# Optimization experiments

Hardware: AMD Instinct MI355X
Metric: run time of the kernel (lower is better)

## Reference

```python
import jax, jax.numpy as jnp
import numpy as np

jax.config.update("jax_enable_x64", True)

P = 2013265921          # NTT-friendly prime 15 * 2**27 + 1 (int64-safe proxy for BLS12-377 Fr)
GEN = 31                # generator of the multiplicative group of F_P
LOGN = 22
N = 1 << LOGN           # domain_size
C = 4                   # columns, as in the module docstring example


def _pow_table(base, n):
    """powers[k] = base**k mod P for k in [0, n), built by repeated doubling (vectorized)."""
    pw = np.ones(n, dtype=np.int64)
    cur = base % P
    step = 1
    while step < n:
        hi = min(2 * step, n)
        pw[step:hi] = (pw[:hi - step] * cur) % P
        cur = (cur * cur) % P
        step *= 2
    return pw


def setup_inputs() -> dict:
    key = jax.random.key(0)
    x = jax.random.randint(key, (N, C), 0, P, dtype=jnp.int64)
    omega = pow(GEN, (P - 1) // N, P)          # primitive N-th root of unity
    omega_inv = pow(omega, P - 2, P)           # its inverse (Fermat)
    twiddles = jnp.asarray(_pow_table(omega_inv, N // 2))  # omega_inv**k, k < N/2  (the 'Params' table)
    n_inv = jnp.asarray(pow(N, P - 2, P), dtype=jnp.int64)  # N^{-1} mod P
    return {"input": x, "twiddles": twiddles, "n_inv": n_inv}


def reference(input, twiddles, n_inv):
    """Inverse NTT over F_P, columns transformed independently. Output in natural order."""
    n, c = input.shape
    logn = n.bit_length() - 1
    # bit-reversal permutation indices (static; computed with numpy)
    idx = np.arange(n)
    rev = np.zeros(n, dtype=np.int64)
    for i in range(logn):
        rev = (rev << 1) | ((idx >> i) & 1)
    x = input[rev]
    # iterative Cooley-Tukey butterflies, logn stages
    for s in range(1, logn + 1):
        m = 1 << s
        half = m >> 1
        w = twiddles[:: n // m]                 # [half] = omega_inv**(j * n/m)
        xr = x.reshape(-1, m, c)                # [n/m, m, c]
        lo, hi = xr[:, :half], xr[:, half:]
        t = (w[None, :, None] * hi) % P         # modular twiddle multiply
        x = jnp.concatenate([(lo + t) % P, (lo - t) % P], axis=1).reshape(n, c)
    return (x * n_inv) % P                      # scale by N^{-1}
```

## Files before the change

kernel.cpp:

```cpp
#include <hip/hip_runtime.h>
#include <stdint.h>

static constexpr uint32_t P = 2013265921u;
static constexpr int      LOGM = 11;
static constexpr int      MSZ  = 1 << LOGM;
static constexpr int      NCOL = 4;

__host__ __device__ constexpr uint32_t neg_pinv32() {
    uint32_t x = 1u;
    for (int i = 0; i < 5; ++i) x *= 2u - P * x;
    return 0u - x;
}
static constexpr uint32_t NEG_PINV = neg_pinv32();
static constexpr uint32_t R1 = (uint32_t)(((uint64_t)1 << 32) % P);
static constexpr uint32_t R2 = (uint32_t)(((uint64_t)R1 * R1) % P);

__device__ __forceinline__ uint32_t mont_mul(uint32_t a, uint32_t b) {
    uint64_t t = (uint64_t)a * (uint64_t)b;
    uint32_t m = (uint32_t)t * NEG_PINV;
    uint32_t r = (uint32_t)((t + (uint64_t)m * P) >> 32);
    uint32_t s = r - P;
    return s < r ? s : r;
}
__device__ __forceinline__ uint32_t to_mont(uint32_t a) { return mont_mul(a, R2); }
__device__ __forceinline__ uint32_t add_p(uint32_t a, uint32_t b) {
    uint32_t r = a + b, s = r - P; return s < r ? s : r;
}
__device__ __forceinline__ uint32_t sub_p(uint32_t a, uint32_t b) {
    uint32_t r = a - b, s = r + P; return s < r ? s : r;
}
__device__ __forceinline__ uint4 mm4(uint32_t w, uint4 v) {
    return make_uint4(mont_mul(w, v.x), mont_mul(w, v.y),
                      mont_mul(w, v.z), mont_mul(w, v.w));
}
__device__ __forceinline__ void bf4(uint4& L, uint4& H, uint32_t w) {
    uint4 t = mm4(w, H);
    uint4 l = L;
    L = make_uint4(add_p(l.x, t.x), add_p(l.y, t.y), add_p(l.z, t.z), add_p(l.w, t.w));
    H = make_uint4(sub_p(l.x, t.x), sub_p(l.y, t.y), sub_p(l.z, t.z), sub_p(l.w, t.w));
}

__device__ __forceinline__ int g_sw(int el) {
    return el ^ (((el >> 3) ^ (el >> 6)) & 7);
}
__device__ __forceinline__ int fidx(int el, int c) { return (g_sw(el) << 2) | c; }

__device__ __forceinline__ void radix8(uint4 x[8],
        uint32_t ta, uint32_t tb0, uint32_t tb1,
        uint32_t tc0, uint32_t tc1, uint32_t tc2, uint32_t tc3) {
    bf4(x[0], x[1], ta);  bf4(x[2], x[3], ta);
    bf4(x[4], x[5], ta);  bf4(x[6], x[7], ta);
    bf4(x[0], x[2], tb0); bf4(x[1], x[3], tb1);
    bf4(x[4], x[6], tb0); bf4(x[5], x[7], tb1);
    bf4(x[0], x[4], tc0); bf4(x[1], x[5], tc1);
    bf4(x[2], x[6], tc2); bf4(x[3], x[7], tc3);
}

template <bool PASS2>
__global__ __launch_bounds__(1024, 4) void intt_pass(
        const uint4* __restrict__ src, uint4* __restrict__ dst,
        const uint32_t* __restrict__ tw,
        const uint32_t* __restrict__ ninv_p)
{
    __shared__ uint4    buf[MSZ * NCOL];
    __shared__ uint32_t stab[2048];

    const int      t   = threadIdx.x;
    const int      c4  = t & 3;
    const int      sub = t >> 2;
    const uint32_t bid = blockIdx.x;
    const uint32_t grp = ((bid & 7u) << 6) | (bid >> 3);
    const uint32_t c   = (grp << 2) | (uint32_t)c4;

#pragma unroll
    for (int q = 0; q < 2; ++q) {
        int e = 2 * t + q;
        if (e < 2047) {
            uint32_t ep1 = (uint32_t)e + 1u;
            int sm1 = 31 - __clz((int)ep1);
            uint32_t j = ep1 - (1u << sm1);
            stab[e] = to_mont(tw[j << (21 - sm1)]);
        }
    }

    const uint32_t r8 = __brev((uint32_t)sub) >> 24;
    uint4 x[8];
#pragma unroll
    for (int m = 0; m < 8; ++m) {
        uint32_t r3 = __brev((uint32_t)m) >> 29;
        x[m] = src[((r3 << 8) | r8) * (uint32_t)MSZ + c];
    }
    __syncthreads();

    radix8(x, stab[0], stab[1], stab[2], stab[3], stab[4], stab[5], stab[6]);
#pragma unroll
    for (int m = 0; m < 8; ++m) buf[fidx(8 * sub + m, c4)] = x[m];
    __syncthreads();

    {
        const int L = sub & 7, hi = sub >> 3;
        const int base = (hi << 6) | L;
#pragma unroll
        for (int m = 0; m < 8; ++m) x[m] = buf[fidx(base | (m << 3), c4)];
        radix8(x, stab[7 + L], stab[15 + L], stab[23 + L],
                  stab[31 + L], stab[39 + L], stab[47 + L], stab[55 + L]);
#pragma unroll
        for (int m = 0; m < 8; ++m) buf[fidx(base | (m << 3), c4)] = x[m];
    }
    __syncthreads();

    {
        const int L = sub & 63, hi = sub >> 6;
        const int base = (hi << 9) | L;
#pragma unroll
        for (int m = 0; m < 8; ++m) x[m] = buf[fidx(base | (m << 6), c4)];
        radix8(x, stab[63 + L], stab[127 + L], stab[191 + L],
                  stab[255 + L], stab[319 + L], stab[383 + L], stab[447 + L]);
#pragma unroll
        for (int m = 0; m < 8; ++m) buf[fidx(base | (m << 6), c4)] = x[m];
    }
    __syncthreads();

    uint32_t nm = 0u, s256 = 0u, step512 = 0u, tm0 = 0u;
    if (PASS2) {
        nm = to_mont(*ninv_p);
    } else {
        s256    = to_mont(tw[c << 8]);
        step512 = mont_mul(s256, s256);
        tm0     = to_mont(tw[c * (uint32_t)sub]);
    }
#pragma unroll
    for (int gg = 0; gg < 2; ++gg) {
        const int lo = sub + (gg << 8);
        uint4 y[4];
#pragma unroll
        for (int m = 0; m < 4; ++m) y[m] = buf[fidx(lo | (m << 9), c4)];
        const uint32_t t10  = stab[511 + lo];
        const uint32_t t110 = stab[1023 + lo];
        const uint32_t t111 = stab[1535 + lo];
        bf4(y[0], y[1], t10);  bf4(y[2], y[3], t10);
        bf4(y[0], y[2], t110); bf4(y[1], y[3], t111);

        if (!PASS2) {
            uint32_t tm = tm0;
#pragma unroll
            for (int m = 0; m < 4; ++m) {
                dst[c * (uint32_t)MSZ + (uint32_t)((m << 9) | lo)] = mm4(tm, y[m]);
                tm = mont_mul(tm, step512);
            }
            tm0 = mont_mul(tm0, s256);
        } else {
#pragma unroll
            for (int m = 0; m < 4; ++m)
                dst[(uint32_t)((m << 9) | lo) * (uint32_t)MSZ + c] = mm4(nm, y[m]);
        }
    }
}

extern "C" void kernel_launch(void* const* d_in, const int* in_sizes, int n_in,
                              void* d_out, int out_size, void* d_ws, size_t ws_size,
                              hipStream_t stream)
{
    const uint4*    x    = (const uint4*)d_in[0];
    const uint32_t* tw   = (const uint32_t*)d_in[1];
    const uint32_t* ninv = (const uint32_t*)d_in[2];
    uint4*          out  = (uint4*)d_out;

    intt_pass<false><<<dim3(512), dim3(1024), 0, stream>>>(x, out, tw, ninv);
    intt_pass<true ><<<dim3(512), dim3(1024), 0, stream>>>(out, out, tw, ninv);
}
```

Measured before the change: 209.6 us.

## Halve columns per block, split Montgomery multiply into 32-bit ops, nontemporal final stores

```diff
diff --git a/kernel.cpp b/kernel.cpp
--- a/kernel.cpp
+++ b/kernel.cpp
@@ -4,7 +4,6 @@
 static constexpr uint32_t P = 2013265921u;
 static constexpr int      LOGM = 11;
 static constexpr int      MSZ  = 1 << LOGM;
-static constexpr int      NCOL = 4;
 
 __host__ __device__ constexpr uint32_t neg_pinv32() {
     uint32_t x = 1u;
@@ -16,10 +15,11 @@
 static constexpr uint32_t R2 = (uint32_t)(((uint64_t)R1 * R1) % P);
 
 __device__ __forceinline__ uint32_t mont_mul(uint32_t a, uint32_t b) {
-    uint64_t t = (uint64_t)a * (uint64_t)b;
-    uint32_t m = (uint32_t)t * NEG_PINV;
-    uint32_t r = (uint32_t)((t + (uint64_t)m * P) >> 32);
-    uint32_t s = r - P;
+    uint32_t tlo = a * b;
+    uint32_t thi = __umulhi(a, b);
+    uint32_t m   = tlo * NEG_PINV;
+    uint32_t r   = thi + __umulhi(m, P) + (tlo != 0u);
+    uint32_t s   = r - P;
     return s < r ? s : r;
 }
 __device__ __forceinline__ uint32_t to_mont(uint32_t a) { return mont_mul(a, R2); }
@@ -40,10 +40,16 @@
     H = make_uint4(sub_p(l.x, t.x), sub_p(l.y, t.y), sub_p(l.z, t.z), sub_p(l.w, t.w));
 }
 
+typedef unsigned int u32v4 __attribute__((ext_vector_type(4)));
+__device__ __forceinline__ void nt_store16(uint4* p, uint4 v) {
+    u32v4 w; w.x = v.x; w.y = v.y; w.z = v.z; w.w = v.w;
+    __builtin_nontemporal_store(w, (u32v4*)p);
+}
+
 __device__ __forceinline__ int g_sw(int el) {
     return el ^ (((el >> 3) ^ (el >> 6)) & 7);
 }
-__device__ __forceinline__ int fidx(int el, int c) { return (g_sw(el) << 2) | c; }
+__device__ __forceinline__ int fidx(int el, int c2) { return (g_sw(el) << 1) | c2; }
 
 __device__ __forceinline__ void radix8(uint4 x[8],
         uint32_t ta, uint32_t tb0, uint32_t tb1,
@@ -57,24 +63,24 @@
 }
 
 template <bool PASS2>
-__global__ __launch_bounds__(1024, 4) void intt_pass(
+__global__ __launch_bounds__(512, 4) void intt_pass(
         const uint4* __restrict__ src, uint4* __restrict__ dst,
         const uint32_t* __restrict__ tw,
         const uint32_t* __restrict__ ninv_p)
 {
-    __shared__ uint4    buf[MSZ * NCOL];
+    __shared__ uint4    buf[MSZ * 2];
     __shared__ uint32_t stab[2048];
 
     const int      t   = threadIdx.x;
-    const int      c4  = t & 3;
-    const int      sub = t >> 2;
+    const int      c2  = t & 1;
+    const int      sub = t >> 1;
     const uint32_t bid = blockIdx.x;
-    const uint32_t grp = ((bid & 7u) << 6) | (bid >> 3);
-    const uint32_t c   = (grp << 2) | (uint32_t)c4;
+    const uint32_t grp = ((bid & 7u) << 7) | (bid >> 3);
+    const uint32_t c   = (grp << 1) | (uint32_t)c2;
 
 #pragma unroll
-    for (int q = 0; q < 2; ++q) {
-        int e = 2 * t + q;
+    for (int q = 0; q < 4; ++q) {
+        int e = t + (q << 9);
         if (e < 2047) {
             uint32_t ep1 = (uint32_t)e + 1u;
             int sm1 = 31 - __clz((int)ep1);
@@ -94,18 +100,18 @@
 
     radix8(x, stab[0], stab[1], stab[2], stab[3], stab[4], stab[5], stab[6]);
 #pragma unroll
-    for (int m = 0; m < 8; ++m) buf[fidx(8 * sub + m, c4)] = x[m];
+    for (int m = 0; m < 8; ++m) buf[fidx(8 * sub + m, c2)] = x[m];
     __syncthreads();
 
     {
         const int L = sub & 7, hi = sub >> 3;
         const int base = (hi << 6) | L;
 #pragma unroll
-        for (int m = 0; m < 8; ++m) x[m] = buf[fidx(base | (m << 3), c4)];
+        for (int m = 0; m < 8; ++m) x[m] = buf[fidx(base | (m << 3), c2)];
         radix8(x, stab[7 + L], stab[15 + L], stab[23 + L],
                   stab[31 + L], stab[39 + L], stab[47 + L], stab[55 + L]);
 #pragma unroll
-        for (int m = 0; m < 8; ++m) buf[fidx(base | (m << 3), c4)] = x[m];
+        for (int m = 0; m < 8; ++m) buf[fidx(base | (m << 3), c2)] = x[m];
     }
     __syncthreads();
 
@@ -113,11 +119,11 @@
         const int L = sub & 63, hi = sub >> 6;
         const int base = (hi << 9) | L;
 #pragma unroll
-        for (int m = 0; m < 8; ++m) x[m] = buf[fidx(base | (m << 6), c4)];
+        for (int m = 0; m < 8; ++m) x[m] = buf[fidx(base | (m << 6), c2)];
         radix8(x, stab[63 + L], stab[127 + L], stab[191 + L],
                   stab[255 + L], stab[319 + L], stab[383 + L], stab[447 + L]);
 #pragma unroll
-        for (int m = 0; m < 8; ++m) buf[fidx(base | (m << 6), c4)] = x[m];
+        for (int m = 0; m < 8; ++m) buf[fidx(base | (m << 6), c2)] = x[m];
     }
     __syncthreads();
 
@@ -134,7 +140,7 @@
         const int lo = sub + (gg << 8);
         uint4 y[4];
 #pragma unroll
-        for (int m = 0; m < 4; ++m) y[m] = buf[fidx(lo | (m << 9), c4)];
+        for (int m = 0; m < 4; ++m) y[m] = buf[fidx(lo | (m << 9), c2)];
         const uint32_t t10  = stab[511 + lo];
         const uint32_t t110 = stab[1023 + lo];
         const uint32_t t111 = stab[1535 + lo];
@@ -152,7 +158,8 @@
         } else {
 #pragma unroll
             for (int m = 0; m < 4; ++m)
-                dst[(uint32_t)((m << 9) | lo) * (uint32_t)MSZ + c] = mm4(nm, y[m]);
+                nt_store16(&dst[(uint32_t)((m << 9) | lo) * (uint32_t)MSZ + c],
+                           mm4(nm, y[m]));
         }
     }
 }
@@ -166,6 +173,6 @@
     const uint32_t* ninv = (const uint32_t*)d_in[2];
     uint4*          out  = (uint4*)d_out;
 
-    intt_pass<false><<<dim3(512), dim3(1024), 0, stream>>>(x, out, tw, ninv);
-    intt_pass<true ><<<dim3(512), dim3(1024), 0, stream>>>(out, out, tw, ninv);
+    intt_pass<false><<<dim3(1024), dim3(512), 0, stream>>>(x, out, tw, ninv);
+    intt_pass<true ><<<dim3(1024), dim3(512), 0, stream>>>(out, out, tw, ninv);
 }
```

After: 218.9 us. 4.4% more time.

## Use Shoup precomputed twiddle multiplication and specialize trivial first-stage butterflies

Applied to the files above, without the earlier changes.

```diff
diff --git a/kernel.cpp b/kernel.cpp
--- a/kernel.cpp
+++ b/kernel.cpp
@@ -16,13 +16,21 @@
 static constexpr uint32_t R2 = (uint32_t)(((uint64_t)R1 * R1) % P);
 
 __device__ __forceinline__ uint32_t mont_mul(uint32_t a, uint32_t b) {
-    uint64_t t = (uint64_t)a * (uint64_t)b;
-    uint32_t m = (uint32_t)t * NEG_PINV;
-    uint32_t r = (uint32_t)((t + (uint64_t)m * P) >> 32);
-    uint32_t s = r - P;
+    uint32_t tlo = a * b;
+    uint32_t thi = __umulhi(a, b);
+    uint32_t m   = tlo * NEG_PINV;
+    uint32_t r   = thi + __umulhi(m, P) + (tlo != 0u);
+    uint32_t s   = r - P;
     return s < r ? s : r;
 }
 __device__ __forceinline__ uint32_t to_mont(uint32_t a) { return mont_mul(a, R2); }
+
+__device__ __forceinline__ uint32_t shoup_mul(uint32_t w, uint32_t wp, uint32_t x) {
+    uint32_t q = __umulhi(wp, x);
+    uint32_t t = w * x - q * P;
+    uint32_t s = t - P;
+    return s < t ? s : t;
+}
 __device__ __forceinline__ uint32_t add_p(uint32_t a, uint32_t b) {
     uint32_t r = a + b, s = r - P; return s < r ? s : r;
 }
@@ -33,37 +41,49 @@
     return make_uint4(mont_mul(w, v.x), mont_mul(w, v.y),
                       mont_mul(w, v.z), mont_mul(w, v.w));
 }
-__device__ __forceinline__ void bf4(uint4& L, uint4& H, uint32_t w) {
-    uint4 t = mm4(w, H);
+__device__ __forceinline__ void bf4_sh(uint4& L, uint4& H, uint2 w) {
+    uint4 t = make_uint4(shoup_mul(w.x, w.y, H.x), shoup_mul(w.x, w.y, H.y),
+                         shoup_mul(w.x, w.y, H.z), shoup_mul(w.x, w.y, H.w));
     uint4 l = L;
     L = make_uint4(add_p(l.x, t.x), add_p(l.y, t.y), add_p(l.z, t.z), add_p(l.w, t.w));
     H = make_uint4(sub_p(l.x, t.x), sub_p(l.y, t.y), sub_p(l.z, t.z), sub_p(l.w, t.w));
 }
+__device__ __forceinline__ void bf4_mont(uint4& L, uint4& H, uint32_t wm) {
+    uint4 t = mm4(wm, H);
+    uint4 l = L;
+    L = make_uint4(add_p(l.x, t.x), add_p(l.y, t.y), add_p(l.z, t.z), add_p(l.w, t.w));
+    H = make_uint4(sub_p(l.x, t.x), sub_p(l.y, t.y), sub_p(l.z, t.z), sub_p(l.w, t.w));
+}
+__device__ __forceinline__ void bf4_triv(uint4& L, uint4& H) {
+    uint4 l = L, h = H;
+    L = make_uint4(add_p(l.x, h.x), add_p(l.y, h.y), add_p(l.z, h.z), add_p(l.w, h.w));
+    H = make_uint4(sub_p(l.x, h.x), sub_p(l.y, h.y), sub_p(l.z, h.z), sub_p(l.w, h.w));
+}
 
 __device__ __forceinline__ int g_sw(int el) {
     return el ^ (((el >> 3) ^ (el >> 6)) & 7);
 }
-__device__ __forceinline__ int fidx(int el, int c) { return (g_sw(el) << 2) | c; }
-
-__device__ __forceinline__ void radix8(uint4 x[8],
-        uint32_t ta, uint32_t tb0, uint32_t tb1,
-        uint32_t tc0, uint32_t tc1, uint32_t tc2, uint32_t tc3) {
-    bf4(x[0], x[1], ta);  bf4(x[2], x[3], ta);
-    bf4(x[4], x[5], ta);  bf4(x[6], x[7], ta);
-    bf4(x[0], x[2], tb0); bf4(x[1], x[3], tb1);
-    bf4(x[4], x[6], tb0); bf4(x[5], x[7], tb1);
-    bf4(x[0], x[4], tc0); bf4(x[1], x[5], tc1);
-    bf4(x[2], x[6], tc2); bf4(x[3], x[7], tc3);
+__device__ __forceinline__ int fidx(int el, int c4) { return (g_sw(el) << 2) | c4; }
+
+__device__ __forceinline__ void radix8_sh(uint4 x[8],
+        uint2 ta, uint2 tb0, uint2 tb1,
+        uint2 tc0, uint2 tc1, uint2 tc2, uint2 tc3) {
+    bf4_sh(x[0], x[1], ta);  bf4_sh(x[2], x[3], ta);
+    bf4_sh(x[4], x[5], ta);  bf4_sh(x[6], x[7], ta);
+    bf4_sh(x[0], x[2], tb0); bf4_sh(x[1], x[3], tb1);
+    bf4_sh(x[4], x[6], tb0); bf4_sh(x[5], x[7], tb1);
+    bf4_sh(x[0], x[4], tc0); bf4_sh(x[1], x[5], tc1);
+    bf4_sh(x[2], x[6], tc2); bf4_sh(x[3], x[7], tc3);
 }
 
 template <bool PASS2>
-__global__ __launch_bounds__(1024, 4) void intt_pass(
+__global__ __launch_bounds__(1024, 2) void intt_pass(
         const uint4* __restrict__ src, uint4* __restrict__ dst,
         const uint32_t* __restrict__ tw,
         const uint32_t* __restrict__ ninv_p)
 {
-    __shared__ uint4    buf[MSZ * NCOL];
-    __shared__ uint32_t stab[2048];
+    __shared__ uint4 buf[MSZ * NCOL];
+    __shared__ uint2 stab[2048];
 
     const int      t   = threadIdx.x;
     const int      c4  = t & 3;
@@ -72,14 +92,16 @@
     const uint32_t grp = ((bid & 7u) << 6) | (bid >> 3);
     const uint32_t c   = (grp << 2) | (uint32_t)c4;
 
+    uint32_t wv[2]; int ev[2];
 #pragma unroll
     for (int q = 0; q < 2; ++q) {
-        int e = 2 * t + q;
+        int e = t + (q << 10);
+        ev[q] = e;
         if (e < 2047) {
             uint32_t ep1 = (uint32_t)e + 1u;
             int sm1 = 31 - __clz((int)ep1);
             uint32_t j = ep1 - (1u << sm1);
-            stab[e] = to_mont(tw[j << (21 - sm1)]);
+            wv[q] = tw[j << (21 - sm1)];
         }
     }
 
@@ -90,9 +112,26 @@
         uint32_t r3 = __brev((uint32_t)m) >> 29;
         x[m] = src[((r3 << 8) | r8) * (uint32_t)MSZ + c];
     }
-    __syncthreads();
-
-    radix8(x, stab[0], stab[1], stab[2], stab[3], stab[4], stab[5], stab[6]);
+
+#pragma unroll
+    for (int q = 0; q < 2; ++q) {
+        if (ev[q] < 2047) {
+            uint32_t w  = wv[q];
+            uint32_t wp = (uint32_t)((((uint64_t)w) << 32) / P);
+            stab[ev[q]] = make_uint2(w, wp);
+        }
+    }
+
+    const uint32_t u1 = to_mont(tw[1u << 20]);
+    const uint32_t u2 = to_mont(tw[1u << 19]);
+    const uint32_t u3 = to_mont(tw[3u << 19]);
+
+    bf4_triv(x[0], x[1]);  bf4_triv(x[2], x[3]);
+    bf4_triv(x[4], x[5]);  bf4_triv(x[6], x[7]);
+    bf4_triv(x[0], x[2]);  bf4_mont(x[1], x[3], u1);
+    bf4_triv(x[4], x[6]);  bf4_mont(x[5], x[7], u1);
+    bf4_triv(x[0], x[4]);  bf4_mont(x[1], x[5], u2);
+    bf4_mont(x[2], x[6], u1); bf4_mont(x[3], x[7], u3);
 #pragma unroll
     for (int m = 0; m < 8; ++m) buf[fidx(8 * sub + m, c4)] = x[m];
     __syncthreads();
@@ -102,8 +141,8 @@
         const int base = (hi << 6) | L;
 #pragma unroll
         for (int m = 0; m < 8; ++m) x[m] = buf[fidx(base | (m << 3), c4)];
-        radix8(x, stab[7 + L], stab[15 + L], stab[23 + L],
-                  stab[31 + L], stab[39 + L], stab[47 + L], stab[55 + L]);
+        radix8_sh(x, stab[7 + L], stab[15 + L], stab[23 + L],
+                     stab[31 + L], stab[39 + L], stab[47 + L], stab[55 + L]);
 #pragma unroll
         for (int m = 0; m < 8; ++m) buf[fidx(base | (m << 3), c4)] = x[m];
     }
@@ -114,8 +153,8 @@
         const int base = (hi << 9) | L;
 #pragma unroll
         for (int m = 0; m < 8; ++m) x[m] = buf[fidx(base | (m << 6), c4)];
-        radix8(x, stab[63 + L], stab[127 + L], stab[191 + L],
-                  stab[255 + L], stab[319 + L], stab[383 + L], stab[447 + L]);
+        radix8_sh(x, stab[63 + L], stab[127 + L], stab[191 + L],
+                     stab[255 + L], stab[319 + L], stab[383 + L], stab[447 + L]);
 #pragma unroll
         for (int m = 0; m < 8; ++m) buf[fidx(base | (m << 6), c4)] = x[m];
     }
@@ -135,11 +174,11 @@
         uint4 y[4];
 #pragma unroll
         for (int m = 0; m < 4; ++m) y[m] = buf[fidx(lo | (m << 9), c4)];
-        const uint32_t t10  = stab[511 + lo];
-        const uint32_t t110 = stab[1023 + lo];
-        const uint32_t t111 = stab[1535 + lo];
-        bf4(y[0], y[1], t10);  bf4(y[2], y[3], t10);
-        bf4(y[0], y[2], t110); bf4(y[1], y[3], t111);
+        const uint2 t10  = stab[511 + lo];
+        const uint2 t110 = stab[1023 + lo];
+        const uint2 t111 = stab[1535 + lo];
+        bf4_sh(y[0], y[1], t10);  bf4_sh(y[2], y[3], t10);
+        bf4_sh(y[0], y[2], t110); bf4_sh(y[1], y[3], t111);
 
         if (!PASS2) {
             uint32_t tm = tm0;
```

Result: faster. 201.2 us (-4.0%).
